# Kernel tuning notes

Hardware: AMD Instinct MI355X
Metric: run time of the kernel (lower is better)

Reference implementation:

```python
import jax, jax.numpy as jnp
import numpy as np

S, B, IN, H, DFF, OUT, L, NHEAD, WINDOW = 2048, 4, 64, 1024, 1024, 64, 3, 4, 4
EPS = 1e-5


def _layer_norm(x, scale, bias):
    m = jnp.mean(x, axis=-1, keepdims=True)
    v = jnp.var(x, axis=-1, keepdims=True)
    return (x - m) * jax.lax.rsqrt(v + EPS) * scale + bias


def setup_inputs() -> dict:
    key = jax.random.key(0)
    ks = jax.random.split(key, 12)
    s = 0.02
    return {
        "src": jax.random.normal(ks[0], (S, B, IN), dtype=jnp.float32),
        "Wenc": jax.random.normal(ks[1], (H, IN), dtype=jnp.float32) * s,
        "benc": jnp.zeros((H,), jnp.float32),
        "Wqkv": jax.random.normal(ks[2], (L, 3 * H, H), dtype=jnp.float32) * s,
        "bqkv": jnp.zeros((L, 3 * H), jnp.float32),
        "Wo": jax.random.normal(ks[3], (L, H, H), dtype=jnp.float32) * s,
        "bo": jnp.zeros((L, H), jnp.float32),
        "W1": jax.random.normal(ks[4], (L, DFF, H), dtype=jnp.float32) * s,
        "b1": jnp.zeros((L, DFF), jnp.float32),
        "W2": jax.random.normal(ks[5], (L, H, DFF), dtype=jnp.float32) * s,
        "b2": jnp.zeros((L, H), jnp.float32),
        "ln1_s": jnp.ones((L, H), jnp.float32),
        "ln1_b": jnp.zeros((L, H), jnp.float32),
        "ln2_s": jnp.ones((L, H), jnp.float32),
        "ln2_b": jnp.zeros((L, H), jnp.float32),
        "Wout": jax.random.normal(ks[6], (OUT, H), dtype=jnp.float32) * s,
        "bout": jnp.zeros((OUT,), jnp.float32),
    }


def _banded_mask(sz):
    # triu(1) masked + lower-band (j < i-4) masked => allowed: i-4 <= j <= i
    i = jnp.arange(sz)[:, None]
    j = jnp.arange(sz)[None, :]
    allowed = (j <= i) & (j >= i - WINDOW)
    return jnp.where(allowed, 0.0, -1e9).astype(jnp.float32)


def reference(src, Wenc, benc, Wqkv, bqkv, Wo, bo, W1, b1, W2, b2,
              ln1_s, ln1_b, ln2_s, ln2_b, Wout, bout):
    dh = H // NHEAD
    mask = _banded_mask(src.shape[0])  # [S, S]
    x = src @ Wenc.T + benc  # [S, B, H]  (NOTE: pos_encoder is never applied in the source)

    def layer(x, p):
        Wqkv_, bqkv_, Wo_, bo_, W1_, b1_, W2_, b2_, s1, g1, s2, g2 = p
        qkv = x @ Wqkv_.T + bqkv_  # [S, B, 3H]
        q, k, v = jnp.split(qkv, 3, axis=-1)
        sS, sB = x.shape[0], x.shape[1]
        q = q.reshape(sS, sB, NHEAD, dh)
        k = k.reshape(sS, sB, NHEAD, dh)
        v = v.reshape(sS, sB, NHEAD, dh)
        scores = jnp.einsum('sbhd,tbhd->bhst', q, k) / jnp.sqrt(jnp.float32(dh))
        scores = scores + mask  # broadcast over [b, h]
        attn = jax.nn.softmax(scores, axis=-1)
        ctx = jnp.einsum('bhst,tbhd->sbhd', attn, v).reshape(sS, sB, H)
        attn_out = ctx @ Wo_.T + bo_
        x = _layer_norm(x + attn_out, s1, g1)  # post-norm (PyTorch default)
        ff = jax.nn.relu(x @ W1_.T + b1_) @ W2_.T + b2_
        x = _layer_norm(x + ff, s2, g2)
        return x, None

    x, _ = jax.lax.scan(layer, x, (Wqkv, bqkv, Wo, bo, W1, b1, W2, b2,
                                   ln1_s, ln1_b, ln2_s, ln2_b))
    return x @ Wout.T + bout  # [S, B, OUT]
```

## Files before the change

kernel.cpp:

```cpp
#include <hip/hip_runtime.h>
#include <hip/hip_bf16.h>

#define S_LEN   2048
#define BATCH   4
#define IN_DIM  64
#define H_DIM   1024
#define DFF_DIM 1024
#define OUT_DIM 64
#define NLAYER  3
#define NHEADS  4
#define DHEAD   256
#define WIN     4
#define ROWS    (S_LEN*BATCH)
#define QKV_LD  (3*H_DIM)


typedef __bf16 bf16x8 __attribute__((ext_vector_type(8)));
typedef float  f32x4  __attribute__((ext_vector_type(4)));

__device__ __forceinline__ float bfbits2f(unsigned int u) {
  union { unsigned int i; float f; } c; c.i = u << 16; return c.f;
}
__device__ __forceinline__ unsigned short f2bfbits(float f) {
  __hip_bfloat16 h = __float2bfloat16(f);
  return __builtin_bit_cast(unsigned short, h);
}

__global__ __launch_bounds__(256)
void cvt_k(const float* __restrict__ in, __hip_bfloat16* __restrict__ out, int n)
{
  int i = blockIdx.x * 256 + threadIdx.x;
  if (i < n) out[i] = __float2bfloat16(in[i]);
}

template<int RELU, int OUTF32>
__global__ __launch_bounds__(256, 2)
void gemm_bt(const __hip_bfloat16* __restrict__ A, int lda,
             const __hip_bfloat16* __restrict__ B,
             const float* __restrict__ bias,
             void* __restrict__ Cp, int ldc,
             int M, int N, int K)
{
  __shared__ __align__(16) __hip_bfloat16 As[128 * 32];
  __shared__ __align__(16) __hip_bfloat16 Bs[128 * 32];

  const int tid  = threadIdx.x;
  const int lane = tid & 63;
  const int wave = tid >> 6;
  const int quad = lane >> 4;
  const int l16  = lane & 15;
  const int m0 = blockIdx.y * 128;
  const int n0 = blockIdx.x * 128;
  const int wr = (wave >> 1) * 64;
  const int wc = (wave & 1) * 64;

  const int i0  = tid;
  const int i1  = tid + 256;
  const int ar0 = i0 >> 2, ac0 = (i0 & 3) * 8;
  const int ar1 = i1 >> 2, ac1 = (i1 & 3) * 8;
  const int br0 = min(n0 + ar0, N - 1);
  const int br1 = min(n0 + ar1, N - 1);

  f32x4 acc[4][4] = {};

  for (int k0 = 0; k0 < K; k0 += 32) {
    uint4 va0 = *(const uint4*)(A + (size_t)(m0 + ar0) * lda + k0 + ac0);
    uint4 va1 = *(const uint4*)(A + (size_t)(m0 + ar1) * lda + k0 + ac1);
    uint4 vb0 = *(const uint4*)(B + (size_t)br0 * K + k0 + ac0);
    uint4 vb1 = *(const uint4*)(B + (size_t)br1 * K + k0 + ac1);
    __syncthreads();
    *(uint4*)&As[i0 * 8] = va0;
    *(uint4*)&As[i1 * 8] = va1;
    *(uint4*)&Bs[i0 * 8] = vb0;
    *(uint4*)&Bs[i1 * 8] = vb1;
    __syncthreads();

    bf16x8 af[4], bfr[4];
#pragma unroll
    for (int i = 0; i < 4; i++)
      af[i] = *(const bf16x8*)&As[(wr + i * 16 + l16) * 32 + quad * 8];
#pragma unroll
    for (int j = 0; j < 4; j++)
      bfr[j] = *(const bf16x8*)&Bs[(wc + j * 16 + l16) * 32 + quad * 8];
#pragma unroll
    for (int i = 0; i < 4; i++)
#pragma unroll
      for (int j = 0; j < 4; j++)
        acc[i][j] = __builtin_amdgcn_mfma_f32_16x16x32_bf16(af[i], bfr[j], acc[i][j], 0, 0, 0);
  }

#pragma unroll
  for (int j = 0; j < 4; j++) {
    int col = n0 + wc + j * 16 + l16;
    if (col < N) {
      float bv = bias[col];
#pragma unroll
      for (int i = 0; i < 4; i++) {
        int row = m0 + wr + i * 16 + quad * 4;
#pragma unroll
        for (int r = 0; r < 4; r++) {
          float v = acc[i][j][r] + bv;
          if (RELU) v = fmaxf(v, 0.f);
          if (OUTF32) ((float*)Cp)[(size_t)(row + r) * ldc + col] = v;
          else ((__hip_bfloat16*)Cp)[(size_t)(row + r) * ldc + col] = __float2bfloat16(v);
        }
      }
    }
  }
}

__global__ __launch_bounds__(256)
void attn_k(__hip_bfloat16* __restrict__ qkv)
{
  const int gw   = (blockIdx.x << 2) + (threadIdx.x >> 6);
  const int lane = threadIdx.x & 63;
  const int h = gw & (NHEADS - 1);
  const int b = (gw >> 2) & (BATCH - 1);
  const int s = gw >> 4;
  const size_t hoff = (size_t)h * DHEAD + (lane << 2);

  float q0, q1, q2, q3;
  {
    uint2 t = *(const uint2*)(qkv + (size_t)(s * BATCH + b) * QKV_LD + hoff);
    q0 = bfbits2f(t.x & 0xffff); q1 = bfbits2f(t.x >> 16);
    q2 = bfbits2f(t.y & 0xffff); q3 = bfbits2f(t.y >> 16);
  }

  float sc[WIN + 1];
#pragma unroll
  for (int jj = 0; jj <= WIN; jj++) {
    int j = s - WIN + jj;
    float v = -1e30f;
    if (j >= 0) {
      uint2 t = *(const uint2*)(qkv + (size_t)(j * BATCH + b) * QKV_LD + H_DIM + hoff);
      float p = q0 * bfbits2f(t.x & 0xffff) + q1 * bfbits2f(t.x >> 16)
              + q2 * bfbits2f(t.y & 0xffff) + q3 * bfbits2f(t.y >> 16);
#pragma unroll
      for (int o = 32; o; o >>= 1) p += __shfl_xor(p, o);
      v = p * 0.0625f;
    }
    sc[jj] = v;
  }

  float mx = sc[0];
#pragma unroll
  for (int jj = 1; jj <= WIN; jj++) mx = fmaxf(mx, sc[jj]);
  float p[WIN + 1], den = 0.f;
#pragma unroll
  for (int jj = 0; jj <= WIN; jj++) { p[jj] = __expf(sc[jj] - mx); den += p[jj]; }

  float a0 = 0.f, a1 = 0.f, a2 = 0.f, a3 = 0.f;
#pragma unroll
  for (int jj = 0; jj <= WIN; jj++) {
    int j = s - WIN + jj;
    if (j >= 0) {
      uint2 t = *(const uint2*)(qkv + (size_t)(j * BATCH + b) * QKV_LD + 2 * H_DIM + hoff);
      a0 += p[jj] * bfbits2f(t.x & 0xffff); a1 += p[jj] * bfbits2f(t.x >> 16);
      a2 += p[jj] * bfbits2f(t.y & 0xffff); a3 += p[jj] * bfbits2f(t.y >> 16);
    }
  }
  float rl = 1.f / den;
  uint2 o;
  o.x = (unsigned)f2bfbits(a0 * rl) | ((unsigned)f2bfbits(a1 * rl) << 16);
  o.y = (unsigned)f2bfbits(a2 * rl) | ((unsigned)f2bfbits(a3 * rl) << 16);
  *(uint2*)(qkv + (size_t)(s * BATCH + b) * QKV_LD + hoff) = o;
}

__global__ __launch_bounds__(256)
void add_ln_k(__hip_bfloat16* __restrict__ x, const __hip_bfloat16* __restrict__ y, int ys,
              const float* __restrict__ g, const float* __restrict__ be)
{
  const int row = blockIdx.x, tid = threadIdx.x;
  const size_t base = (size_t)row * H_DIM + tid * 4;
  uint2 xv = *(const uint2*)(x + base);
  uint2 yv = *(const uint2*)(y + (size_t)row * ys + tid * 4);
  float t0 = bfbits2f(xv.x & 0xffff) + bfbits2f(yv.x & 0xffff);
  float t1 = bfbits2f(xv.x >> 16)    + bfbits2f(yv.x >> 16);
  float t2 = bfbits2f(xv.y & 0xffff) + bfbits2f(yv.y & 0xffff);
  float t3 = bfbits2f(xv.y >> 16)    + bfbits2f(yv.y >> 16);
  float s  = t0 + t1 + t2 + t3;
  float ss = t0 * t0 + t1 * t1 + t2 * t2 + t3 * t3;
#pragma unroll
  for (int o = 32; o; o >>= 1) { s += __shfl_down(s, o); ss += __shfl_down(ss, o); }
  __shared__ float rs[4], rss[4];
  if ((tid & 63) == 0) { rs[tid >> 6] = s; rss[tid >> 6] = ss; }
  __syncthreads();
  float S  = rs[0] + rs[1] + rs[2] + rs[3];
  float SS = rss[0] + rss[1] + rss[2] + rss[3];
  const float inv = 1.f / (float)H_DIM;
  float mean = S * inv;
  float var  = SS * inv - mean * mean;
  float rstd = rsqrtf(var + 1e-5f);
  float4 gv = *(const float4*)(g + tid * 4);
  float4 bv = *(const float4*)(be + tid * 4);
  float o0 = (t0 - mean) * rstd * gv.x + bv.x;
  float o1 = (t1 - mean) * rstd * gv.y + bv.y;
  float o2 = (t2 - mean) * rstd * gv.z + bv.z;
  float o3 = (t3 - mean) * rstd * gv.w + bv.w;
  uint2 ob;
  ob.x = (unsigned)f2bfbits(o0) | ((unsigned)f2bfbits(o1) << 16);
  ob.y = (unsigned)f2bfbits(o2) | ((unsigned)f2bfbits(o3) << 16);
  *(uint2*)(x + base) = ob;
}

extern "C" void kernel_launch(void* const* d_in, const int* in_sizes, int n_in,
                              void* d_out, int out_size, void* d_ws, size_t ws_size,
                              hipStream_t stream) {
  const float* src   = (const float*)d_in[0];
  const float* Wenc  = (const float*)d_in[1];
  const float* benc  = (const float*)d_in[2];
  const float* Wqkv  = (const float*)d_in[3];
  const float* bqkv  = (const float*)d_in[4];
  const float* Wo    = (const float*)d_in[5];
  const float* bo    = (const float*)d_in[6];
  const float* W1    = (const float*)d_in[7];
  const float* b1    = (const float*)d_in[8];
  const float* W2    = (const float*)d_in[9];
  const float* b2    = (const float*)d_in[10];
  const float* ln1s  = (const float*)d_in[11];
  const float* ln1b  = (const float*)d_in[12];
  const float* ln2s  = (const float*)d_in[13];
  const float* ln2b  = (const float*)d_in[14];
  const float* Wout  = (const float*)d_in[15];
  const float* bout  = (const float*)d_in[16];

  char* ws = (char*)d_ws;
  __hip_bfloat16* WB   = (__hip_bfloat16*)ws;
  __hip_bfloat16* srcb = WB;
  __hip_bfloat16* wenc = WB + 524288;
  __hip_bfloat16* wqkv = WB + 589824;
  __hip_bfloat16* wo   = WB + 10027008;
  __hip_bfloat16* w1   = WB + 13172736;
  __hip_bfloat16* w2   = WB + 16318464;
  __hip_bfloat16* wout = WB + 19464192;
  __hip_bfloat16* xb  = (__hip_bfloat16*)(ws + (size_t)40 * 1048576);
  __hip_bfloat16* qkv = (__hip_bfloat16*)(ws + (size_t)56 * 1048576);
  __hip_bfloat16* ctxp = qkv;
  __hip_bfloat16* ybuf = qkv + H_DIM;
  __hip_bfloat16* hbuf = qkv + 2 * H_DIM;

  const dim3 blk(256);
  #define CVT(inp, outp, n) cvt_k<<<dim3(((n) + 255) / 256), blk, 0, stream>>>(inp, outp, n)

  CVT(src,  srcb, 524288);
  CVT(Wenc, wenc, 65536);
  CVT(Wqkv, wqkv, 9437184);
  CVT(Wo,   wo,   3145728);
  CVT(W1,   w1,   3145728);
  CVT(W2,   w2,   3145728);
  CVT(Wout, wout, 65536);

  gemm_bt<0, 0><<<dim3(H_DIM / 128, ROWS / 128), blk, 0, stream>>>(
      srcb, IN_DIM, wenc, benc, xb, H_DIM, ROWS, H_DIM, IN_DIM);

  for (int l = 0; l < NLAYER; l++) {
    gemm_bt<0, 0><<<dim3(QKV_LD / 128, ROWS / 128), blk, 0, stream>>>(
        xb, H_DIM, wqkv + (size_t)l * QKV_LD * H_DIM, bqkv + l * QKV_LD,
        qkv, QKV_LD, ROWS, QKV_LD, H_DIM);
    attn_k<<<dim3(ROWS * NHEADS / 4), blk, 0, stream>>>(qkv);
    gemm_bt<0, 0><<<dim3(H_DIM / 128, ROWS / 128), blk, 0, stream>>>(
        ctxp, QKV_LD, wo + (size_t)l * H_DIM * H_DIM, bo + l * H_DIM,
        ybuf, QKV_LD, ROWS, H_DIM, H_DIM);
    add_ln_k<<<dim3(ROWS), blk, 0, stream>>>(xb, ybuf, QKV_LD, ln1s + l * H_DIM, ln1b + l * H_DIM);
    gemm_bt<1, 0><<<dim3(DFF_DIM / 128, ROWS / 128), blk, 0, stream>>>(
        xb, H_DIM, w1 + (size_t)l * DFF_DIM * H_DIM, b1 + l * DFF_DIM,
        hbuf, QKV_LD, ROWS, DFF_DIM, H_DIM);
    gemm_bt<0, 0><<<dim3(H_DIM / 128, ROWS / 128), blk, 0, stream>>>(
        hbuf, QKV_LD, w2 + (size_t)l * H_DIM * DFF_DIM, b2 + l * H_DIM,
        ybuf, QKV_LD, ROWS, H_DIM, DFF_DIM);
    add_ln_k<<<dim3(ROWS), blk, 0, stream>>>(xb, ybuf, QKV_LD, ln2s + l * H_DIM, ln2b + l * H_DIM);
  }

  gemm_bt<0, 1><<<dim3(1, ROWS / 128), blk, 0, stream>>>(
      xb, H_DIM, wout, bout, d_out, OUT_DIM, ROWS, OUT_DIM, H_DIM);
}
```

Baseline: 835.8 us.

## Load GEMM tiles directly to LDS with XOR swizzle; vectorize fp32-to-bf16 conversion

The GEMM now uses global_load_lds to copy A/B tiles straight into shared memory, skipping the register staging step. An XOR swizzle on the k-chunk index is meant to reduce LDS bank conflicts when the fragments are read back. The barrier is moved to the end of each k-step. Separately, the conversion kernel now processes four floats per thread with vector loads and stores. Risks are that the direct-to-LDS load must wait on vmcnt before the barrier, and the loop still has no prefetch or double buffering.

```diff
diff --git a/kernel.cpp b/kernel.cpp
--- a/kernel.cpp
+++ b/kernel.cpp
@@ -26,11 +26,22 @@
   return __builtin_bit_cast(unsigned short, h);
 }
 
+__device__ __forceinline__ void g2l16(const void* g, void* l) {
+  __builtin_amdgcn_global_load_lds((__attribute__((address_space(1))) void*)g,
+                                   (__attribute__((address_space(3))) void*)l,
+                                   16, 0, 0);
+}
+
 __global__ __launch_bounds__(256)
 void cvt_k(const float* __restrict__ in, __hip_bfloat16* __restrict__ out, int n)
 {
-  int i = blockIdx.x * 256 + threadIdx.x;
-  if (i < n) out[i] = __float2bfloat16(in[i]);
+  int i = (blockIdx.x * 256 + threadIdx.x) * 4;
+  if (i >= n) return;
+  float4 v = *(const float4*)(in + i);
+  uint2 o;
+  o.x = (unsigned)f2bfbits(v.x) | ((unsigned)f2bfbits(v.y) << 16);
+  o.y = (unsigned)f2bfbits(v.z) | ((unsigned)f2bfbits(v.w) << 16);
+  *(uint2*)(out + i) = o;
 }
 
 template<int RELU, int OUTF32>
@@ -54,39 +65,43 @@
   const int wr = (wave >> 1) * 64;
   const int wc = (wave & 1) * 64;
 
-  const int i0  = tid;
-  const int i1  = tid + 256;
-  const int ar0 = i0 >> 2, ac0 = (i0 & 3) * 8;
-  const int ar1 = i1 >> 2, ac1 = (i1 & 3) * 8;
+  const int p0  = wave * 64 + lane;
+  const int p1  = p0 + 256;
+  const int ar0 = p0 >> 2, ac0 = (((p0 & 3) ^ ((ar0 >> 1) & 3))) * 8;
+  const int ar1 = p1 >> 2, ac1 = (((p1 & 3) ^ ((ar1 >> 1) & 3))) * 8;
   const int br0 = min(n0 + ar0, N - 1);
   const int br1 = min(n0 + ar1, N - 1);
+  __hip_bfloat16* lA0 = &As[(wave * 64)       * 8];
+  __hip_bfloat16* lA1 = &As[(wave * 64 + 256) * 8];
+  __hip_bfloat16* lB0 = &Bs[(wave * 64)       * 8];
+  __hip_bfloat16* lB1 = &Bs[(wave * 64 + 256) * 8];
 
   f32x4 acc[4][4] = {};
 
   for (int k0 = 0; k0 < K; k0 += 32) {
-    uint4 va0 = *(const uint4*)(A + (size_t)(m0 + ar0) * lda + k0 + ac0);
-    uint4 va1 = *(const uint4*)(A + (size_t)(m0 + ar1) * lda + k0 + ac1);
-    uint4 vb0 = *(const uint4*)(B + (size_t)br0 * K + k0 + ac0);
-    uint4 vb1 = *(const uint4*)(B + (size_t)br1 * K + k0 + ac1);
+    g2l16(A + (size_t)(m0 + ar0) * lda + k0 + ac0, lA0);
+    g2l16(A + (size_t)(m0 + ar1) * lda + k0 + ac1, lA1);
+    g2l16(B + (size_t)br0 * K + k0 + ac0, lB0);
+    g2l16(B + (size_t)br1 * K + k0 + ac1, lB1);
     __syncthreads();
-    *(uint4*)&As[i0 * 8] = va0;
-    *(uint4*)&As[i1 * 8] = va1;
-    *(uint4*)&Bs[i0 * 8] = vb0;
-    *(uint4*)&Bs[i1 * 8] = vb1;
-    __syncthreads();
 
     bf16x8 af[4], bfr[4];
 #pragma unroll
-    for (int i = 0; i < 4; i++)
-      af[i] = *(const bf16x8*)&As[(wr + i * 16 + l16) * 32 + quad * 8];
-#pragma unroll
-    for (int j = 0; j < 4; j++)
-      bfr[j] = *(const bf16x8*)&Bs[(wc + j * 16 + l16) * 32 + quad * 8];
+    for (int i = 0; i < 4; i++) {
+      const int row = wr + i * 16 + l16;
+      af[i] = *(const bf16x8*)&As[row * 32 + ((quad ^ ((row >> 1) & 3)) * 8)];
+    }
+#pragma unroll
+    for (int j = 0; j < 4; j++) {
+      const int row = wc + j * 16 + l16;
+      bfr[j] = *(const bf16x8*)&Bs[row * 32 + ((quad ^ ((row >> 1) & 3)) * 8)];
+    }
 #pragma unroll
     for (int i = 0; i < 4; i++)
 #pragma unroll
       for (int j = 0; j < 4; j++)
         acc[i][j] = __builtin_amdgcn_mfma_f32_16x16x32_bf16(af[i], bfr[j], acc[i][j], 0, 0, 0);
+    __syncthreads();
   }
 
 #pragma unroll
@@ -240,7 +255,7 @@
   __hip_bfloat16* hbuf = qkv + 2 * H_DIM;
 
   const dim3 blk(256);
-  #define CVT(inp, outp, n) cvt_k<<<dim3(((n) + 255) / 256), blk, 0, stream>>>(inp, outp, n)
+  #define CVT(inp, outp, n) cvt_k<<<dim3(((n) / 4 + 255) / 256), blk, 0, stream>>>(inp, outp, n)
 
   CVT(src,  srcb, 524288);
   CVT(Wenc, wenc, 65536);
```

Measured after the change: 797.1 us. -4.6%, faster.
